# Performance work log

Measured on AMD Instinct MI355X. Metric: run time of the kernel, lower is better.

The kernel has to match this reference:

```python
import jax, jax.numpy as jnp
import numpy as np

N_EMBED = 256
N_HEADS = 4
HEAD_SIZE = N_EMBED // N_HEADS  # 64
BLOCK_SIZE = 768
LN_EPS = 1e-5


def layer_norm(x, g, b):
    mu = jnp.mean(x, axis=-1, keepdims=True)
    var = jnp.var(x, axis=-1, keepdims=True)
    return (x - mu) * jax.lax.rsqrt(var + LN_EPS) * g + b


def setup_inputs() -> dict:
    key = jax.random.key(0)
    ks = jax.random.split(key, 12)
    B, T, C, H, hs = 32, BLOCK_SIZE, N_EMBED, N_HEADS, HEAD_SIZE
    s_in = 1.0 / np.sqrt(C)
    s_ff = 1.0 / np.sqrt(4 * C)
    return {
        "x": jax.random.normal(ks[0], (B, T, C), jnp.float32),
        # per-head projections, stacked: [H, C, hs]
        "Wq": jax.random.normal(ks[1], (H, C, hs), jnp.float32) * s_in,
        "Wk": jax.random.normal(ks[2], (H, C, hs), jnp.float32) * s_in,
        "Wv": jax.random.normal(ks[3], (H, C, hs), jnp.float32) * s_in,
        "Wo": jax.random.normal(ks[4], (C, C), jnp.float32) * s_in,
        "bo": jnp.zeros((C,), jnp.float32),
        "W1": jax.random.normal(ks[5], (C, 4 * C), jnp.float32) * s_in,
        "b1": jnp.zeros((4 * C,), jnp.float32),
        "W2": jax.random.normal(ks[6], (4 * C, C), jnp.float32) * s_ff,
        "b2": jnp.zeros((C,), jnp.float32),
        "g1": jnp.ones((C,), jnp.float32),
        "be1": jnp.zeros((C,), jnp.float32),
        "g2": jnp.ones((C,), jnp.float32),
        "be2": jnp.zeros((C,), jnp.float32),
    }


def reference(x, Wq, Wk, Wv, Wo, bo, W1, b1, W2, b2, g1, be1, g2, be2):
    B, T, C = x.shape
    # --- multi-head causal self-attention (pre-LN) ---
    h = layer_norm(x, g1, be1)
    q = jnp.einsum("btc,hcd->bhtd", h, Wq)
    k = jnp.einsum("btc,hcd->bhtd", h, Wk)
    v = jnp.einsum("btc,hcd->bhtd", h, Wv)
    scores = jnp.einsum("bhtd,bhsd->bhts", q, k) * (HEAD_SIZE ** -0.5)
    causal = jnp.tril(jnp.ones((T, T), bool))
    scores = jnp.where(causal, scores, -jnp.inf)
    attn = jax.nn.softmax(scores, axis=-1)  # dropout = identity (eval)
    o = jnp.einsum("bhts,bhsd->bhtd", attn, v)
    o = o.transpose(0, 2, 1, 3).reshape(B, T, C)  # concat heads
    x = x + o @ Wo + bo
    # --- feed-forward (pre-LN) ---
    h2 = layer_norm(x, g2, be2)
    x = x + jax.nn.relu(h2 @ W1 + b1) @ W2 + b2
    return x
```

## Files before the change

### kernel.cpp

```cpp
#include <hip/hip_runtime.h>
#include <stdint.h>

using short8   = __attribute__((ext_vector_type(8))) short;
using f32x4    = __attribute__((ext_vector_type(4))) float;
using ushort4v = __attribute__((ext_vector_type(4))) unsigned short;
using uint2v   = __attribute__((ext_vector_type(2))) unsigned int;

#define CSC  0.1803368801111f
#define FIXC 20.0f

#define WAITLG()   asm volatile("s_waitcnt lgkmcnt(0)" ::: "memory")
#define WAITVM(n)  asm volatile("s_waitcnt vmcnt(" #n ")" ::: "memory")
#define BAR()      __builtin_amdgcn_s_barrier()

__device__ __forceinline__ unsigned short f2bf(float f) {
    unsigned int u = __builtin_bit_cast(unsigned int, f);
    u += 0x7FFFu + ((u >> 16) & 1u);
    return (unsigned short)(u >> 16);
}
__device__ __forceinline__ float bf2f(unsigned short s) {
    unsigned int u = ((unsigned int)s) << 16;
    return __builtin_bit_cast(float, u);
}
__device__ __forceinline__ unsigned pk2bf(float a, float b) {
    unsigned r;
    asm("v_cvt_pk_bf16_f32 %0, %1, %2" : "=v"(r) : "v"(a), "v"(b));
    return r;
}

__device__ __forceinline__ void gload16(const void* g, void* l) {
    __builtin_amdgcn_global_load_lds(
        (const __attribute__((address_space(1))) void*)(uintptr_t)g,
        (__attribute__((address_space(3))) void*)(unsigned)(uintptr_t)l,
        16, 0, 0);
}

__device__ __forceinline__ uint2v ln_row_pk(f32x4 v, f32x4 gv, f32x4 bvv) {
    float s  = v[0] + v[1] + v[2] + v[3];
    float s2 = v[0]*v[0] + v[1]*v[1] + v[2]*v[2] + v[3]*v[3];
    for (int m = 1; m < 64; m <<= 1) {
        s  += __shfl_xor(s,  m, 64);
        s2 += __shfl_xor(s2, m, 64);
    }
    float mu  = s * (1.0f / 256.0f);
    float var = s2 * (1.0f / 256.0f) - mu * mu;
    float rs  = rsqrtf(var + 1e-5f);
    float r0 = (v[0] - mu) * rs * gv[0] + bvv[0];
    float r1 = (v[1] - mu) * rs * gv[1] + bvv[1];
    float r2 = (v[2] - mu) * rs * gv[2] + bvv[2];
    float r3 = (v[3] - mu) * rs * gv[3] + bvv[3];
    uint2v u; u[0] = pk2bf(r0, r1); u[1] = pk2bf(r2, r3);
    return u;
}

__global__ __launch_bounds__(256) void prep_k(const float* __restrict__ x, const float* __restrict__ g1,
                                              const float* __restrict__ be1, unsigned short* __restrict__ h,
                                              const float* __restrict__ Wq, const float* __restrict__ Wk,
                                              const float* __restrict__ Wv, const float* __restrict__ Wo,
                                              const float* __restrict__ W1, const float* __restrict__ W2,
                                              unsigned short* __restrict__ wpackT, unsigned short* __restrict__ woT,
                                              unsigned short* __restrict__ w1T, unsigned short* __restrict__ w2T) {
    __shared__ float t[64][65];
    if (blockIdx.x >= 192) {
        int row  = (blockIdx.x - 192) * 4 + (threadIdx.x >> 6);
        int lane = threadIdx.x & 63;
        f32x4 v = *(const f32x4*)(x + (size_t)row * 256 + lane * 4);
        f32x4 gv = *(const f32x4*)(g1 + lane * 4);
        f32x4 bv = *(const f32x4*)(be1 + lane * 4);
        uint2v u = ln_row_pk(v, gv, bv);
        *(uint2v*)(h + (size_t)row * 256 + lane * 4) = u;
        return;
    }
    const int bid = blockIdx.x;
    const float* in; unsigned short* out;
    int R, C, r0, c0;
    if (bid < 48) {
        int z = bid >> 2, cx = bid & 3;
        int qkv = z >> 2, hh = z & 3;
        in = ((qkv == 0) ? Wq : (qkv == 1) ? Wk : Wv) + (size_t)hh * 256 * 64;
        out = wpackT + (size_t)(qkv * 256 + hh * 64) * 256;
        R = 256; C = 64; r0 = cx * 64; c0 = 0;
    } else if (bid < 64) {
        int tt = bid - 48;
        in = Wo; out = woT; R = 256; C = 256; r0 = (tt >> 2) * 64; c0 = (tt & 3) * 64;
    } else if (bid < 128) {
        int tt = bid - 64;
        in = W1; out = w1T; R = 256; C = 1024; r0 = (tt & 3) * 64; c0 = (tt >> 2) * 64;
    } else {
        int tt = bid - 128;
        in = W2; out = w2T; R = 1024; C = 256; r0 = (tt & 15) * 64; c0 = (tt >> 4) * 64;
    }
    const int tx = threadIdx.x & 63, ty = threadIdx.x >> 6;
    #pragma unroll
    for (int i = 0; i < 64; i += 4)
        t[i + ty][tx] = in[(size_t)(r0 + i + ty) * C + c0 + tx];
    __syncthreads();
    #pragma unroll
    for (int i = 0; i < 64; i += 4)
        out[(size_t)(c0 + i + ty) * R + r0 + tx] = f2bf(t[tx][i + ty]);
}

__global__ __launch_bounds__(256) void qkv_k(const unsigned short* __restrict__ h,
                                             const unsigned short* __restrict__ wpackT,
                                             unsigned short* __restrict__ qk,
                                             unsigned short* __restrict__ vT) {
    __shared__ unsigned short As[2][128 * 64];
    __shared__ unsigned short Bs[2][128 * 64];
    const int tid  = threadIdx.x;
    const int lane = tid & 63;
    const int w    = tid >> 6;
    const int wm   = w >> 1, wn = w & 1;
    const int l15  = lane & 15, l4 = lane >> 4;
    const int bid  = blockIdx.x;

    const unsigned short *A, *BT;
    unsigned short* outp;
    int bm, bn, N;
    float qsc = 1.0f;
    if (bid < 768) {
        const int xcd = bid & 7, i = bid >> 3;
        bm = xcd * 24 + (i >> 2);
        bn = i & 3;
        A = h; BT = wpackT; outp = qk; N = 512;
        if (bn < 2) qsc = CSC;
    } else {
        const int t = bid - 768;
        const int xcd = t & 7, j = t >> 3;
        bn = xcd * 24 + (j >> 1);
        bm = j & 1;
        A = wpackT + 512 * 256; BT = h; outp = vT; N = 24576;
    }
    const int K = 256;

    f32x4 acc[4][4] = {};

    const size_t K2 = (size_t)K * 2;
    const int i0   = w * 4096 + lane * 16;
    const int row0 = i0 >> 7;
    const int cb0  = (i0 & 127) ^ ((row0 & 7) << 4);
    const char* aSrc = (const char*)A  + ((size_t)(bm * 128 + row0)) * K2 + cb0;
    const char* bSrc = (const char*)BT + ((size_t)(bn * 128 + row0)) * K2 + cb0;

    auto stage = [&](int t, int buf) {
        #pragma unroll
        for (int c = 0; c < 4; ++c) {
            gload16(aSrc + (size_t)t * 128 + (size_t)c * 8 * K2,
                    (char*)&As[buf][0] + w * 4096 + c * 1024);
            gload16(bSrc + (size_t)t * 128 + (size_t)c * 8 * K2,
                    (char*)&Bs[buf][0] + w * 4096 + c * 1024);
        }
    };

    stage(0, 0);
    stage(1, 1);

    #pragma unroll
    for (int t = 0; t < 4; ++t) {
        WAITLG();
        if (t < 3) { WAITVM(8); } else { WAITVM(0); }
        BAR();
        const char* AsB = (const char*)&As[t & 1][0];
        const char* BsB = (const char*)&Bs[t & 1][0];
        #pragma unroll
        for (int kf = 0; kf < 2; ++kf) {
            int kb = kf * 64 + l4 * 16;
            short8 af[4], bfr[4];
            #pragma unroll
            for (int mf = 0; mf < 4; ++mf) {
                int row = wm * 64 + mf * 16 + l15;
                af[mf] = *(const short8*)(AsB + ((row * 128 + kb) ^ ((row & 7) << 4)));
            }
            #pragma unroll
            for (int nf = 0; nf < 4; ++nf) {
                int row = wn * 64 + nf * 16 + l15;
                bfr[nf] = *(const short8*)(BsB + ((row * 128 + kb) ^ ((row & 7) << 4)));
            }
            #pragma unroll
            for (int mf = 0; mf < 4; ++mf)
                #pragma unroll
                for (int nf = 0; nf < 4; ++nf)
                    acc[mf][nf] = __builtin_amdgcn_mfma_f32_16x16x32_bf16(af[mf], bfr[nf], acc[mf][nf], 0, 0, 0);
        }
        BAR();
        if (t + 2 < 4) stage(t + 2, t & 1);
    }

    #pragma unroll
    for (int nf = 0; nf < 4; ++nf) {
        int col = bn * 128 + wn * 64 + nf * 16 + l15;
        #pragma unroll
        for (int mf = 0; mf < 4; ++mf) {
            int row0o = bm * 128 + wm * 64 + mf * 16 + l4 * 4;
            size_t off = (size_t)row0o * N + col;
            unsigned p01 = pk2bf(acc[mf][nf][0] * qsc, acc[mf][nf][1] * qsc);
            unsigned p23 = pk2bf(acc[mf][nf][2] * qsc, acc[mf][nf][3] * qsc);
            outp[off]                 = (unsigned short)p01;
            outp[off + (size_t)N]     = (unsigned short)(p01 >> 16);
            outp[off + (size_t)N * 2] = (unsigned short)p23;
            outp[off + (size_t)N * 3] = (unsigned short)(p23 >> 16);
        }
    }
}

__global__ __launch_bounds__(256) void oproj_k(const unsigned short* __restrict__ A,
                                               const unsigned short* __restrict__ BT,
                                               unsigned short* __restrict__ outp,
                                               const float* __restrict__ bias,
                                               const float* __restrict__ resid) {
    __shared__ unsigned short As[2][128 * 64];
    __shared__ unsigned short Bs[2][128 * 64];
    const int tid  = threadIdx.x;
    const int lane = tid & 63;
    const int w    = tid >> 6;
    const int wm   = w >> 1, wn = w & 1;
    const int bm   = blockIdx.y, bn = blockIdx.x;
    const int l15  = lane & 15, l4 = lane >> 4;
    const int N = 256;

    f32x4 acc[4][4] = {};

    const size_t K2 = 512;
    const int i0   = w * 4096 + lane * 16;
    const int row0 = i0 >> 7;
    const int cb0  = (i0 & 127) ^ ((row0 & 7) << 4);
    const char* aSrc = (const char*)A  + ((size_t)(bm * 128 + row0)) * K2 + cb0;
    const char* bSrc = (const char*)BT + ((size_t)(bn * 128 + row0)) * K2 + cb0;

    auto stage = [&](int t, int buf) {
        #pragma unroll
        for (int c = 0; c < 4; ++c) {
            gload16(aSrc + (size_t)t * 128 + (size_t)c * 8 * K2,
                    (char*)&As[buf][0] + w * 4096 + c * 1024);
            gload16(bSrc + (size_t)t * 128 + (size_t)c * 8 * K2,
                    (char*)&Bs[buf][0] + w * 4096 + c * 1024);
        }
    };

    stage(0, 0);
    stage(1, 1);

    #pragma unroll
    for (int t = 0; t < 4; ++t) {
        WAITLG();
        if (t < 3) { WAITVM(8); } else { WAITVM(0); }
        BAR();
        const char* AsB = (const char*)&As[t & 1][0];
        const char* BsB = (const char*)&Bs[t & 1][0];
        #pragma unroll
        for (int kf = 0; kf < 2; ++kf) {
            int kb = kf * 64 + l4 * 16;
            short8 af[4], bfr[4];
            #pragma unroll
            for (int mf = 0; mf < 4; ++mf) {
                int row = wm * 64 + mf * 16 + l15;
                af[mf] = *(const short8*)(AsB + ((row * 128 + kb) ^ ((row & 7) << 4)));
            }
            #pragma unroll
            for (int nf = 0; nf < 4; ++nf) {
                int row = wn * 64 + nf * 16 + l15;
                bfr[nf] = *(const short8*)(BsB + ((row * 128 + kb) ^ ((row & 7) << 4)));
            }
            #pragma unroll
            for (int mf = 0; mf < 4; ++mf)
                #pragma unroll
                for (int nf = 0; nf < 4; ++nf)
                    acc[mf][nf] = __builtin_amdgcn_mfma_f32_16x16x32_bf16(af[mf], bfr[nf], acc[mf][nf], 0, 0, 0);
        }
        BAR();
        if (t + 2 < 4) stage(t + 2, t & 1);
    }

    #pragma unroll
    for (int nf = 0; nf < 4; ++nf) {
        int col = bn * 128 + wn * 64 + nf * 16 + l15;
        float bv = bias[col];
        #pragma unroll
        for (int mf = 0; mf < 4; ++mf) {
            int row0o = bm * 128 + wm * 64 + mf * 16 + l4 * 4;
            size_t off = (size_t)row0o * N + col;
            float v[4];
            #pragma unroll
            for (int r = 0; r < 4; ++r)
                v[r] = acc[mf][nf][r] + bv + resid[off + (size_t)r * N];
            unsigned p01 = pk2bf(v[0], v[1]), p23 = pk2bf(v[2], v[3]);
            outp[off]                 = (unsigned short)p01;
            outp[off + (size_t)N]     = (unsigned short)(p01 >> 16);
            outp[off + (size_t)N * 2] = (unsigned short)p23;
            outp[off + (size_t)N * 3] = (unsigned short)(p23 >> 16);
        }
    }
}

__global__ __launch_bounds__(512, 2) void ff_fused(const unsigned short* __restrict__ x1b,
                                                   const float* __restrict__ g2,
                                                   const float* __restrict__ be2,
                                                   const unsigned short* __restrict__ w1T,
                                                   const unsigned short* __restrict__ w2T,
                                                   const float* __restrict__ b1,
                                                   const float* __restrict__ b2,
                                                   float* __restrict__ out) {
    __shared__ __align__(16) char smem[151552];
    const int tid = threadIdx.x, lane = tid & 63, w = tid >> 6;
    const int l15 = lane & 15, l4 = lane >> 4;
    const int wm = w >> 2, wn = w & 3;
    const int r0 = blockIdx.x * 96;

    {
        f32x4 gv = *(const f32x4*)(g2 + lane * 4);
        f32x4 bv = *(const f32x4*)(be2 + lane * 4);
        const int ks = lane >> 4, colb = (lane & 15) * 8;
        #pragma unroll
        for (int it = 0; it < 12; ++it) {
            int row = it * 8 + w;
            ushort4v u4 = *(const ushort4v*)(x1b + (size_t)(r0 + row) * 256 + lane * 4);
            f32x4 v;
            #pragma unroll
            for (int q = 0; q < 4; ++q) v[q] = bf2f(u4[q]);
            uint2v u = ln_row_pk(v, gv, bv);
            *(uint2v*)(smem + ks * 12288 + row * 128 + (colb ^ ((row & 7) << 4))) = u;
        }
    }
    WAITLG(); BAR();

    short8 hfr[3][4][2];
    #pragma unroll
    for (int mf = 0; mf < 3; ++mf) {
        const int row = wm * 48 + mf * 16 + l15;
        #pragma unroll
        for (int ks = 0; ks < 4; ++ks)
            #pragma unroll
            for (int kf = 0; kf < 2; ++kf) {
                const int kb = kf * 64 + l4 * 16;
                hfr[mf][ks][kf] = *(const short8*)(smem + ks * 12288
                                    + ((row * 128 + kb) ^ ((row & 7) << 4)));
            }
    }
    WAITLG(); BAR();

    auto stage_w1 = [&](int c, int buf) {
        const char* wb = (const char*)w1T + (size_t)(c * 64) * 512;
        #pragma unroll
        for (int g = 0; g < 4; ++g) {
            int j = g * 8192 + tid * 16;
            int ks = j >> 13, row = (j >> 7) & 63, cb = j & 127;
            gload16(wb + (size_t)row * 512 + ks * 128 + (cb ^ ((row & 7) << 4)),
                    smem + buf * 32768 + j);
        }
    };
    auto stage_w2 = [&](int c, int buf) {
        const char* wb = (const char*)w2T + (size_t)c * 128;
        #pragma unroll
        for (int g = 0; g < 4; ++g) {
            int j = g * 8192 + tid * 16;
            int row = j >> 7, cb = j & 127;
            gload16(wb + (size_t)row * 2048 + (cb ^ ((row & 7) << 4)),
                    smem + 65536 + buf * 32768 + j);
        }
    };

    gload16((const char*)b1 + (tid & 255) * 16, smem + 143360 + tid * 16);
    stage_w1(0, 0);
    stage_w2(0, 0);
    stage_w1(1, 1);

    const float* sB1f = (const float*)(smem + 143360);
    f32x4 oacc[3][4] = {};

    for (int c = 0; c < 16; ++c) {
        WAITLG();
        if (c < 15) { WAITVM(8); } else { WAITVM(4); }
        BAR();
        if (c + 1 < 16) stage_w2(c + 1, (c + 1) & 1);

        const char* W1B = smem + (c & 1) * 32768;
        f32x4 aacc[3] = {};
        __builtin_amdgcn_s_setprio(1);
        #pragma unroll
        for (int ks = 0; ks < 4; ++ks) {
            #pragma unroll
            for (int kf = 0; kf < 2; ++kf) {
                const int kb = kf * 64 + l4 * 16;
                int row = wn * 16 + l15;
                short8 wf = *(const short8*)(W1B + ks * 8192
                              + ((row * 128 + kb) ^ ((row & 7) << 4)));
                #pragma unroll
                for (int mf = 0; mf < 3; ++mf)
                    aacc[mf] = __builtin_amdgcn_mfma_f32_16x16x32_bf16(wf, hfr[mf][ks][kf], aacc[mf], 0, 0, 0);
            }
        }
        __builtin_amdgcn_s_setprio(0);
        #pragma unroll
        for (int mf = 0; mf < 3; ++mf) {
            int nl = wn * 16 + l4 * 4;
            f32x4 bv = *(const f32x4*)(sB1f + c * 64 + nl);
            float v0 = aacc[mf][0] + bv[0]; v0 = v0 > 0.0f ? v0 : 0.0f;
            float v1 = aacc[mf][1] + bv[1]; v1 = v1 > 0.0f ? v1 : 0.0f;
            float v2 = aacc[mf][2] + bv[2]; v2 = v2 > 0.0f ? v2 : 0.0f;
            float v3 = aacc[mf][3] + bv[3]; v3 = v3 > 0.0f ? v3 : 0.0f;
            uint2v u; u[0] = pk2bf(v0, v1); u[1] = pk2bf(v2, v3);
            int m = wm * 48 + mf * 16 + l15;
            *(uint2v*)(smem + 131072 + ((m * 128 + nl * 2) ^ ((m & 7) << 4))) = u;
        }

        WAITLG();
        if (c < 15) { WAITVM(8); } else { WAITVM(0); }
        BAR();
        if (c + 2 < 16) stage_w1(c + 2, c & 1);

        const char* W2B = smem + 65536 + (c & 1) * 32768;
        __builtin_amdgcn_s_setprio(1);
        #pragma unroll
        for (int kf = 0; kf < 2; ++kf) {
            const int kb = kf * 64 + l4 * 16;
            short8 af[3], wf[4];
            #pragma unroll
            for (int mf = 0; mf < 3; ++mf) {
                int m = wm * 48 + mf * 16 + l15;
                af[mf] = *(const short8*)(smem + 131072 + ((m * 128 + kb) ^ ((m & 7) << 4)));
            }
            #pragma unroll
            for (int nf = 0; nf < 4; ++nf) {
                int n2 = wn * 64 + nf * 16 + l15;
                wf[nf] = *(const short8*)(W2B + ((n2 * 128 + kb) ^ ((n2 & 7) << 4)));
            }
            #pragma unroll
            for (int mf = 0; mf < 3; ++mf)
                #pragma unroll
                for (int nf = 0; nf < 4; ++nf)
                    oacc[mf][nf] = __builtin_amdgcn_mfma_f32_16x16x32_bf16(af[mf], wf[nf], oacc[mf][nf], 0, 0, 0);
        }
        __builtin_amdgcn_s_setprio(0);
    }

    #pragma unroll
    for (int nf = 0; nf < 4; ++nf) {
        const int col = wn * 64 + nf * 16 + l15;
        const float bv = b2[col];
        #pragma unroll
        for (int mf = 0; mf < 3; ++mf) {
            const int row = r0 + wm * 48 + mf * 16 + l4 * 4;
            const size_t off = (size_t)row * 256 + col;
            #pragma unroll
            for (int r = 0; r < 4; ++r)
                out[off + (size_t)r * 256] = oacc[mf][nf][r] + bv + bf2f(x1b[off + (size_t)r * 256]);
        }
    }
}

__global__ __launch_bounds__(256) void attn_k(const unsigned short* __restrict__ qk,
                                              const unsigned short* __restrict__ vT,
                                              unsigned short* __restrict__ o) {
    __shared__ unsigned short Ks[2][64 * 64];
    __shared__ unsigned short Vt[2][64 * 64];
    __shared__ unsigned short Pl[4][16 * 64];
    const int tid = threadIdx.x, lane = tid & 63, w = tid >> 6;
    const int l15 = lane & 15, l4 = lane >> 4;
    const int gid = blockIdx.x;
    const int xcd = gid & 7, slot = gid >> 3;
    const int sl6 = slot / 6;
    const int bh  = xcd * 16 + sl6;
    const int x   = slot - sl6 * 6;
    const int qb1 = x, qb2 = 11 - x;
    const int b = bh >> 2, h = bh & 3;
    const unsigned short* Qb = qk + (size_t)b * 768 * 512 + h * 64;
    const char* Kg = (const char*)(Qb + 256);
    const char* Vg = (const char*)(vT + (size_t)(h * 64) * 24576 + (size_t)b * 768);
    const int t01 = qb1 * 64, t02 = qb2 * 64;
    const int tq1 = t01 + w * 16 + l15;
    const int tq2 = t02 + w * 16 + l15;

    short8 q1f0 = *(const short8*)(Qb + (size_t)tq1 * 512 + l4 * 8);
    short8 q1f1 = *(const short8*)(Qb + (size_t)tq1 * 512 + 32 + l4 * 8);
    short8 q2f0 = *(const short8*)(Qb + (size_t)tq2 * 512 + l4 * 8);
    short8 q2f1 = *(const short8*)(Qb + (size_t)tq2 * 512 + 32 + l4 * 8);

    const int srow = w * 16 + (lane >> 3);
    const int scb  = ((lane & 7) * 16) ^ ((srow & 7) << 4);
    const char* kSrc = Kg + (size_t)srow * 1024 + scb;
    const char* vSrc = Vg + (size_t)srow * 49152 + scb;
    char* kDst0 = (char*)&Ks[0][0] + w * 2048;
    char* vDst0 = (char*)&Vt[0][0] + w * 2048;

    f32x4 oA[4] = {}, oB[4] = {};
    float lsA = 0.0f, lsB = 0.0f;
    unsigned short* Pw = &Pl[w][0];
    const char* KsB;
    const char* VtB;
    int sb = 0;

    auto do_tile = [&](short8 qf0, short8 qf1, f32x4 (&oacc)[4], float& lsum, bool diag, int tq) {
        f32x4 sacc[4] = {};
        __builtin_amdgcn_s_setprio(1);
        #pragma unroll
        for (int kf = 0; kf < 2; ++kf) {
            const int kb = kf * 64 + l4 * 16;
            short8 qf = kf ? qf1 : qf0;
            #pragma unroll
            for (int nf = 0; nf < 4; ++nf) {
                int sr = nf * 16 + l15;
                short8 kfr = *(const short8*)(KsB + ((sr * 128 + kb) ^ ((sr & 7) << 4)));
                sacc[nf] = __builtin_amdgcn_mfma_f32_16x16x32_bf16(kfr, qf, sacc[nf], 0, 0, 0);
            }
        }
        __builtin_amdgcn_s_setprio(0);

        if (diag) {
            #pragma unroll
            for (int nf = 0; nf < 4; ++nf)
                #pragma unroll
                for (int r = 0; r < 4; ++r) {
                    int s = sb * 64 + nf * 16 + l4 * 4 + r;
                    if (s > tq) sacc[nf][r] = -1e30f;
                }
        }
        float psum = 0.0f;
        #pragma unroll
        for (int nf = 0; nf < 4; ++nf) {
            float p0 = __builtin_amdgcn_exp2f(sacc[nf][0] - FIXC);
            float p1 = __builtin_amdgcn_exp2f(sacc[nf][1] - FIXC);
            float p2 = __builtin_amdgcn_exp2f(sacc[nf][2] - FIXC);
            float p3 = __builtin_amdgcn_exp2f(sacc[nf][3] - FIXC);
            psum += (p0 + p1) + (p2 + p3);
            uint2v u; u[0] = pk2bf(p0, p1); u[1] = pk2bf(p2, p3);
            *(uint2v*)((char*)Pw + ((l15 * 128 + nf * 32 + l4 * 8) ^ ((l15 & 7) << 4))) = u;
        }
        psum += __shfl_xor(psum, 16, 64);
        psum += __shfl_xor(psum, 32, 64);
        lsum += psum;

        __builtin_amdgcn_s_setprio(1);
        #pragma unroll
        for (int kf = 0; kf < 2; ++kf) {
            const int kb = kf * 64 + l4 * 16;
            short8 pa = *(const short8*)((const char*)Pw + ((l15 * 128 + kb) ^ ((l15 & 7) << 4)));
            #pragma unroll
            for (int nf = 0; nf < 4; ++nf) {
                int dr = nf * 16 + l15;
                short8 vfr = *(const short8*)(VtB + ((dr * 128 + kb) ^ ((dr & 7) << 4)));
                oacc[nf] = __builtin_amdgcn_mfma_f32_16x16x32_bf16(pa, vfr, oacc[nf], 0, 0, 0);
            }
        }
        __builtin_amdgcn_s_setprio(0);
    };

    gload16(kSrc, kDst0);                 gload16(kSrc + 8 * 1024, kDst0 + 1024);
    gload16(vSrc, vDst0);                 gload16(vSrc + 8 * 49152, vDst0 + 1024);

    for (sb = 0; sb <= qb2; ++sb) {
        const int pb = sb & 1;
        __syncthreads();
        if (sb < qb2) {
            const char* ks = kSrc + (size_t)(sb + 1) * 65536;
            const char* vs = vSrc + (size_t)(sb + 1) * 128;
            char* kd = kDst0 + (pb ^ 1) * 8192;
            char* vd = vDst0 + (pb ^ 1) * 8192;
            gload16(ks, kd);              gload16(ks + 8 * 1024, kd + 1024);
            gload16(vs, vd);              gload16(vs + 8 * 49152, vd + 1024);
        }
        KsB = (const char*)&Ks[0][0] + pb * 8192;
        VtB = (const char*)&Vt[0][0] + pb * 8192;

        do_tile(q2f0, q2f1, oB, lsB, sb == qb2, tq2);
        if (sb <= qb1) do_tile(q1f0, q1f1, oA, lsA, sb == qb1, tq1);
    }

    float liA = 1.0f / lsA, liB = 1.0f / lsB;
    float lrA[4], lrB[4];
    #pragma unroll
    for (int r = 0; r < 4; ++r) {
        lrA[r] = __shfl(liA, l4 * 4 + r, 64);
        lrB[r] = __shfl(liB, l4 * 4 + r, 64);
    }
    const int tA = t01 + w * 16 + l4 * 4;
    const int tB = t02 + w * 16 + l4 * 4;
    unsigned short* oa = o + ((size_t)(b * 768 + tA)) * 256 + h * 64;
    unsigned short* ob = o + ((size_t)(b * 768 + tB)) * 256 + h * 64;
    #pragma unroll
    for (int nf = 0; nf < 4; ++nf) {
        unsigned a01 = pk2bf(oA[nf][0] * lrA[0], oA[nf][1] * lrA[1]);
        unsigned a23 = pk2bf(oA[nf][2] * lrA[2], oA[nf][3] * lrA[3]);
        unsigned b01 = pk2bf(oB[nf][0] * lrB[0], oB[nf][1] * lrB[1]);
        unsigned b23 = pk2bf(oB[nf][2] * lrB[2], oB[nf][3] * lrB[3]);
        oa[nf * 16 + l15]       = (unsigned short)a01;
        oa[256 + nf * 16 + l15] = (unsigned short)(a01 >> 16);
        oa[512 + nf * 16 + l15] = (unsigned short)a23;
        oa[768 + nf * 16 + l15] = (unsigned short)(a23 >> 16);
        ob[nf * 16 + l15]       = (unsigned short)b01;
        ob[256 + nf * 16 + l15] = (unsigned short)(b01 >> 16);
        ob[512 + nf * 16 + l15] = (unsigned short)b23;
        ob[768 + nf * 16 + l15] = (unsigned short)(b23 >> 16);
    }
}

extern "C" void kernel_launch(void* const* d_in, const int* in_sizes, int n_in,
                              void* d_out, int out_size, void* d_ws, size_t ws_size,
                              hipStream_t stream) {
    const float* x   = (const float*)d_in[0];
    const float* Wq  = (const float*)d_in[1];
    const float* Wk  = (const float*)d_in[2];
    const float* Wv  = (const float*)d_in[3];
    const float* Wo  = (const float*)d_in[4];
    const float* bo  = (const float*)d_in[5];
    const float* W1  = (const float*)d_in[6];
    const float* b1  = (const float*)d_in[7];
    const float* W2  = (const float*)d_in[8];
    const float* b2  = (const float*)d_in[9];
    const float* g1  = (const float*)d_in[10];
    const float* be1 = (const float*)d_in[11];
    const float* g2  = (const float*)d_in[12];
    const float* be2 = (const float*)d_in[13];

    char* ws = (char*)d_ws;
    unsigned short* qk_ws  = (unsigned short*)(ws + 0);
    unsigned short* vT_ws  = (unsigned short*)(ws + 25165824);
    unsigned short* o_ws   = (unsigned short*)(ws + 37748736);
    unsigned short* h_ws   = (unsigned short*)(ws + 50331648);
    unsigned short* x1b_ws = (unsigned short*)(ws + 62914560);
    unsigned short* wpackT = (unsigned short*)(ws + 88080384);
    unsigned short* woT    = (unsigned short*)(ws + 88473600);
    unsigned short* w1T    = (unsigned short*)(ws + 88604672);
    unsigned short* w2T    = (unsigned short*)(ws + 89128960);

    prep_k<<<6336, 256, 0, stream>>>(x, g1, be1, h_ws, Wq, Wk, Wv, Wo, W1, W2, wpackT, woT, w1T, w2T);
    qkv_k<<<1152, 256, 0, stream>>>(h_ws, wpackT, qk_ws, vT_ws);
    attn_k<<<768, 256, 0, stream>>>(qk_ws, vT_ws, o_ws);
    oproj_k<<<dim3(2, 192), 256, 0, stream>>>(o_ws, woT, x1b_ws, bo, x);
    ff_fused<<<256, 512, 0, stream>>>(x1b_ws, g2, be2, w1T, w2T, b1, b2, (float*)d_out);
}
```

Measured before the change: 102.2 us.

## Split attention query-block pair across two wave groups in 512-thread blocks

The attention kernel now runs 8 waves per block instead of 4. Each group of 4 waves owns one of the two paired causal query blocks, where before each wave processed both serially, and the K/V tile loads are spread across all 8 waves. This is meant to raise wave-level parallelism and cut per-wave register pressure and serial work. The cost is idle waves in the group with the shorter causal range, plus larger blocks that may reduce how many blocks fit per CU.

```diff
diff --git a/kernel.cpp b/kernel.cpp
--- a/kernel.cpp
+++ b/kernel.cpp
@@ -447,14 +447,16 @@
     }
 }
 
-__global__ __launch_bounds__(256) void attn_k(const unsigned short* __restrict__ qk,
+__global__ __launch_bounds__(512) void attn_k(const unsigned short* __restrict__ qk,
                                               const unsigned short* __restrict__ vT,
                                               unsigned short* __restrict__ o) {
     __shared__ unsigned short Ks[2][64 * 64];
     __shared__ unsigned short Vt[2][64 * 64];
-    __shared__ unsigned short Pl[4][16 * 64];
+    __shared__ unsigned short Pl[8][16 * 64];
     const int tid = threadIdx.x, lane = tid & 63, w = tid >> 6;
     const int l15 = lane & 15, l4 = lane >> 4;
+    const int grp = w >> 2;
+    const int wl  = w & 3;
     const int gid = blockIdx.x;
     const int xcd = gid & 7, slot = gid >> 3;
     const int sl6 = slot / 6;
@@ -465,30 +467,29 @@
     const unsigned short* Qb = qk + (size_t)b * 768 * 512 + h * 64;
     const char* Kg = (const char*)(Qb + 256);
     const char* Vg = (const char*)(vT + (size_t)(h * 64) * 24576 + (size_t)b * 768);
-    const int t01 = qb1 * 64, t02 = qb2 * 64;
-    const int tq1 = t01 + w * 16 + l15;
-    const int tq2 = t02 + w * 16 + l15;
-
-    short8 q1f0 = *(const short8*)(Qb + (size_t)tq1 * 512 + l4 * 8);
-    short8 q1f1 = *(const short8*)(Qb + (size_t)tq1 * 512 + 32 + l4 * 8);
-    short8 q2f0 = *(const short8*)(Qb + (size_t)tq2 * 512 + l4 * 8);
-    short8 q2f1 = *(const short8*)(Qb + (size_t)tq2 * 512 + 32 + l4 * 8);
-
-    const int srow = w * 16 + (lane >> 3);
+
+    const int myqb = grp ? qb1 : qb2;
+    const int t0   = myqb * 64;
+    const int tq   = t0 + wl * 16 + l15;
+
+    short8 qf0 = *(const short8*)(Qb + (size_t)tq * 512 + l4 * 8);
+    short8 qf1 = *(const short8*)(Qb + (size_t)tq * 512 + 32 + l4 * 8);
+
+    const int srow = w * 8 + (lane >> 3);
     const int scb  = ((lane & 7) * 16) ^ ((srow & 7) << 4);
     const char* kSrc = Kg + (size_t)srow * 1024 + scb;
     const char* vSrc = Vg + (size_t)srow * 49152 + scb;
-    char* kDst0 = (char*)&Ks[0][0] + w * 2048;
-    char* vDst0 = (char*)&Vt[0][0] + w * 2048;
-
-    f32x4 oA[4] = {}, oB[4] = {};
-    float lsA = 0.0f, lsB = 0.0f;
+    char* kDst0 = (char*)&Ks[0][0] + w * 1024;
+    char* vDst0 = (char*)&Vt[0][0] + w * 1024;
+
+    f32x4 oacc[4] = {};
+    float lsum = 0.0f;
     unsigned short* Pw = &Pl[w][0];
     const char* KsB;
     const char* VtB;
     int sb = 0;
 
-    auto do_tile = [&](short8 qf0, short8 qf1, f32x4 (&oacc)[4], float& lsum, bool diag, int tq) {
+    auto do_tile = [&](bool diag) {
         f32x4 sacc[4] = {};
         __builtin_amdgcn_s_setprio(1);
         #pragma unroll
@@ -543,52 +544,40 @@
         __builtin_amdgcn_s_setprio(0);
     };
 
-    gload16(kSrc, kDst0);                 gload16(kSrc + 8 * 1024, kDst0 + 1024);
-    gload16(vSrc, vDst0);                 gload16(vSrc + 8 * 49152, vDst0 + 1024);
+    gload16(kSrc, kDst0);
+    gload16(vSrc, vDst0);
 
     for (sb = 0; sb <= qb2; ++sb) {
         const int pb = sb & 1;
         __syncthreads();
         if (sb < qb2) {
-            const char* ks = kSrc + (size_t)(sb + 1) * 65536;
-            const char* vs = vSrc + (size_t)(sb + 1) * 128;
-            char* kd = kDst0 + (pb ^ 1) * 8192;
-            char* vd = vDst0 + (pb ^ 1) * 8192;
-            gload16(ks, kd);              gload16(ks + 8 * 1024, kd + 1024);
-            gload16(vs, vd);              gload16(vs + 8 * 49152, vd + 1024);
+            gload16(kSrc + (size_t)(sb + 1) * 65536, kDst0 + (pb ^ 1) * 8192);
+            gload16(vSrc + (size_t)(sb + 1) * 128,   vDst0 + (pb ^ 1) * 8192);
         }
         KsB = (const char*)&Ks[0][0] + pb * 8192;
         VtB = (const char*)&Vt[0][0] + pb * 8192;
 
-        do_tile(q2f0, q2f1, oB, lsB, sb == qb2, tq2);
-        if (sb <= qb1) do_tile(q1f0, q1f1, oA, lsA, sb == qb1, tq1);
-    }
-
-    float liA = 1.0f / lsA, liB = 1.0f / lsB;
-    float lrA[4], lrB[4];
-    #pragma unroll
-    for (int r = 0; r < 4; ++r) {
-        lrA[r] = __shfl(liA, l4 * 4 + r, 64);
-        lrB[r] = __shfl(liB, l4 * 4 + r, 64);
-    }
-    const int tA = t01 + w * 16 + l4 * 4;
-    const int tB = t02 + w * 16 + l4 * 4;
-    unsigned short* oa = o + ((size_t)(b * 768 + tA)) * 256 + h * 64;
-    unsigned short* ob = o + ((size_t)(b * 768 + tB)) * 256 + h * 64;
+        if (grp == 0) {
+            do_tile(sb == qb2);
+        } else if (sb <= qb1) {
+            do_tile(sb == qb1);
+        }
+    }
+
+    float li = 1.0f / lsum;
+    float lr[4];
+    #pragma unroll
+    for (int r = 0; r < 4; ++r) lr[r] = __shfl(li, l4 * 4 + r, 64);
+    const int tO = t0 + wl * 16 + l4 * 4;
+    unsigned short* op = o + ((size_t)(b * 768 + tO)) * 256 + h * 64;
     #pragma unroll
     for (int nf = 0; nf < 4; ++nf) {
-        unsigned a01 = pk2bf(oA[nf][0] * lrA[0], oA[nf][1] * lrA[1]);
-        unsigned a23 = pk2bf(oA[nf][2] * lrA[2], oA[nf][3] * lrA[3]);
-        unsigned b01 = pk2bf(oB[nf][0] * lrB[0], oB[nf][1] * lrB[1]);
-        unsigned b23 = pk2bf(oB[nf][2] * lrB[2], oB[nf][3] * lrB[3]);
-        oa[nf * 16 + l15]       = (unsigned short)a01;
-        oa[256 + nf * 16 + l15] = (unsigned short)(a01 >> 16);
-        oa[512 + nf * 16 + l15] = (unsigned short)a23;
-        oa[768 + nf * 16 + l15] = (unsigned short)(a23 >> 16);
-        ob[nf * 16 + l15]       = (unsigned short)b01;
-        ob[256 + nf * 16 + l15] = (unsigned short)(b01 >> 16);
-        ob[512 + nf * 16 + l15] = (unsigned short)b23;
-        ob[768 + nf * 16 + l15] = (unsigned short)(b23 >> 16);
+        unsigned p01 = pk2bf(oacc[nf][0] * lr[0], oacc[nf][1] * lr[1]);
+        unsigned p23 = pk2bf(oacc[nf][2] * lr[2], oacc[nf][3] * lr[3]);
+        op[nf * 16 + l15]       = (unsigned short)p01;
+        op[256 + nf * 16 + l15] = (unsigned short)(p01 >> 16);
+        op[512 + nf * 16 + l15] = (unsigned short)p23;
+        op[768 + nf * 16 + l15] = (unsigned short)(p23 >> 16);
     }
 }
 
@@ -623,7 +612,7 @@
 
     prep_k<<<6336, 256, 0, stream>>>(x, g1, be1, h_ws, Wq, Wk, Wv, Wo, W1, W2, wpackT, woT, w1T, w2T);
     qkv_k<<<1152, 256, 0, stream>>>(h_ws, wpackT, qk_ws, vT_ws);
-    attn_k<<<768, 256, 0, stream>>>(qk_ws, vT_ws, o_ws);
+    attn_k<<<768, 512, 0, stream>>>(qk_ws, vT_ws, o_ws);
     oproj_k<<<dim3(2, 192), 256, 0, stream>>>(o_ws, woT, x1b_ws, bo, x);
     ff_fused<<<256, 512, 0, stream>>>(x1b_ws, g2, be2, w1T, w2T, b1, b2, (float*)d_out);
 }
```

Result: slower. 105.7 us (+3.4%).
